# Optimization experiments

Measured on AMD Instinct MI355X. Metric: run time of the kernel, lower is better.

Reference implementation:

```python
import jax, jax.numpy as jnp
import numpy as np

V, E, H, L = 37, 256, 512, 3
B, S = 512, 128


def lstm_layer(x, W_ih, W_hh, b_ih, b_hh):
    # x: [B,S,D_in]; W_ih: [4H,D_in]; W_hh: [4H,H]; PyTorch gate order i,f,g,o
    Bx = x.shape[0]
    Hh = W_hh.shape[1]
    x_proj = jnp.einsum('bsd,gd->bsg', x, W_ih) + b_ih + b_hh  # [B,S,4H]

    def step(carry, xt):
        h, c = carry
        gates = xt + h @ W_hh.T
        i, f, g, o = jnp.split(gates, 4, axis=-1)
        i = jax.nn.sigmoid(i)
        f = jax.nn.sigmoid(f)
        g = jnp.tanh(g)
        o = jax.nn.sigmoid(o)
        c = f * c + i * g
        h = o * jnp.tanh(c)
        return (h, c), h

    init = (jnp.zeros((Bx, Hh), x.dtype), jnp.zeros((Bx, Hh), x.dtype))
    (hT, cT), hs = jax.lax.scan(step, init, jnp.swapaxes(x_proj, 0, 1))
    return jnp.swapaxes(hs, 0, 1), hT, cT


def setup_inputs() -> dict:
    key = jax.random.key(0)
    ks = jax.random.split(key, 16)
    inp = {'tokens': jax.random.randint(ks[0], (B, S), 0, V)}
    inp['embedding'] = jax.random.normal(ks[1], (V, E), jnp.float32) * 0.05
    for l in range(L):
        d_in = E if l == 0 else H
        inp[f'W_ih{l}'] = jax.random.normal(ks[2 + 4 * l], (4 * H, d_in), jnp.float32) * 0.05
        inp[f'W_hh{l}'] = jax.random.normal(ks[3 + 4 * l], (4 * H, H), jnp.float32) * 0.05
        inp[f'b_ih{l}'] = jnp.zeros((4 * H,), jnp.float32)
        inp[f'b_hh{l}'] = jnp.zeros((4 * H,), jnp.float32)
    inp['W_out'] = jax.random.normal(ks[14], (V, H), jnp.float32) * 0.05
    inp['b_out'] = jnp.zeros((V,), jnp.float32)
    return inp


def reference(tokens, embedding, W_ih0, W_hh0, b_ih0, b_hh0,
              W_ih1, W_hh1, b_ih1, b_hh1,
              W_ih2, W_hh2, b_ih2, b_hh2, W_out, b_out):
    x = embedding[tokens]  # [B,S,E]
    hs, cs = [], []
    for (Wi, Wh, bi, bh) in ((W_ih0, W_hh0, b_ih0, b_hh0),
                             (W_ih1, W_hh1, b_ih1, b_hh1),
                             (W_ih2, W_hh2, b_ih2, b_hh2)):
        x, hT, cT = lstm_layer(x, Wi, Wh, bi, bh)
        hs.append(hT)
        cs.append(cT)
    logits = jnp.einsum('bsh,vh->bsv', x, W_out) + b_out  # [B,S,V]
    return logits, jnp.stack(hs), jnp.stack(cs)
```

## Files before the change

kernel.cpp:

```cpp
#include <hip/hip_runtime.h>

typedef __attribute__((ext_vector_type(4))) float f32x4;
typedef __attribute__((ext_vector_type(8))) short bf16x8;

#define DEV __device__ __forceinline__

DEV float b2f(ushort u) { return __uint_as_float(((uint)u) << 16); }
DEV ushort f2b(float f) {
    uint u = __float_as_uint(f);
    return (ushort)((u + 0x7fffu + ((u >> 16) & 1u)) >> 16);
}
DEV float fsig(float x) {
    return __builtin_amdgcn_rcpf(1.f + __builtin_amdgcn_exp2f(-1.4426950408889634f * x));
}
DEV float ftanh(float x) {
    return 1.f - 2.f * __builtin_amdgcn_rcpf(__builtin_amdgcn_exp2f(2.885390081777927f * x) + 1.f);
}
DEV void gload_lds16(const void* g, void* l) {
    __builtin_amdgcn_global_load_lds(
        (const __attribute__((address_space(1))) void*)g,
        (__attribute__((address_space(3))) void*)l, 16, 0, 0);
}
DEV void gload_lds16_l2(const void* g, void* l) {
    __builtin_amdgcn_global_load_lds(
        (const __attribute__((address_space(1))) void*)g,
        (__attribute__((address_space(3))) void*)l, 16, 0, 1);
}
DEV void store_sc_u32(uint* p, uint v) {
    asm volatile("global_store_dword %0, %1, off sc0 sc1" :: "v"(p), "v"(v) : "memory");
}
DEV uint load_sc_u32(const uint* p) {
    uint v;
    asm volatile("global_load_dword %0, %1, off sc0 sc1\n\ts_waitcnt vmcnt(0)"
                 : "=v"(v) : "v"(p) : "memory");
    return v;
}

__global__ void f2b_kernel(const float* __restrict__ s, ushort* __restrict__ d, int n) {
    int i = blockIdx.x * 256 + threadIdx.x;
    if (i < n) d[i] = f2b(s[i]);
}

__global__ __launch_bounds__(256) void embed_kernel(
    const int* __restrict__ tok, const float* __restrict__ emb, ushort* __restrict__ x0) {
    const int nthr = gridDim.x * 256;
    for (int idx = blockIdx.x * 256 + threadIdx.x; idx < 128 * 512 * 32; idx += nthr) {
        const int row = idx >> 5;
        const int g8 = idx & 31;
        const int t = row >> 9, b = row & 511;
        const int tk = tok[b * 128 + t];
        const float* ep = emb + (size_t)tk * 256 + g8 * 8;
        float4 a = *(const float4*)ep;
        float4 c = *(const float4*)(ep + 4);
        uint4 o;
        o.x = (uint)f2b(a.x) | ((uint)f2b(a.y) << 16);
        o.y = (uint)f2b(a.z) | ((uint)f2b(a.w) << 16);
        o.z = (uint)f2b(c.x) | ((uint)f2b(c.y) << 16);
        o.w = (uint)f2b(c.z) | ((uint)f2b(c.w) << 16);
        *(uint4*)(x0 + (size_t)row * 256 + g8 * 8) = o;
    }
}

__global__ __launch_bounds__(256) void gemm_bias_kernel(
    const ushort* __restrict__ A, const ushort* __restrict__ Bw,
    const float* __restrict__ bias0, const float* __restrict__ bias1,
    ushort* __restrict__ C, int M, int N, int K) {
    __shared__ ushort la[128 * 32];
    __shared__ ushort lb[128 * 32];
    const int tid = threadIdx.x;
    const int wave = tid >> 6, lane = tid & 63;
    const int ntn = N >> 7;
    const int tm = blockIdx.x / ntn, tn = blockIdx.x % ntn;
    const int m0 = tm << 7, n0 = tn << 7;
    const int wm = (wave >> 1) * 64, wn = (wave & 1) * 64;
    f32x4 acc[4][4] = {};
    const int nks = K >> 5;
    const int srow = tid >> 2, scol = (tid & 3) * 8;
    for (int ks = 0; ks < nks; ++ks) {
        const int k0 = ks << 5;
#pragma unroll
        for (int r = 0; r < 2; ++r) {
            gload_lds16(A + (size_t)(m0 + r * 64 + srow) * K + k0 + scol, &la[r * 2048 + wave * 512]);
            gload_lds16(Bw + (size_t)(n0 + r * 64 + srow) * K + k0 + scol, &lb[r * 2048 + wave * 512]);
        }
        __syncthreads();
        bf16x8 af[4], bfr[4];
#pragma unroll
        for (int i = 0; i < 4; ++i)
            af[i] = *(const bf16x8*)&la[(wm + i * 16 + (lane & 15)) * 32 + (lane >> 4) * 8];
#pragma unroll
        for (int i = 0; i < 4; ++i)
            bfr[i] = *(const bf16x8*)&lb[(wn + i * 16 + (lane & 15)) * 32 + (lane >> 4) * 8];
#pragma unroll
        for (int mi = 0; mi < 4; ++mi)
#pragma unroll
            for (int ni = 0; ni < 4; ++ni)
                acc[mi][ni] = __builtin_amdgcn_mfma_f32_16x16x32_bf16(af[mi], bfr[ni], acc[mi][ni], 0, 0, 0);
        __syncthreads();
    }
#pragma unroll
    for (int mi = 0; mi < 4; ++mi) {
        int row = m0 + wm + mi * 16 + ((lane >> 4) << 2);
#pragma unroll
        for (int j = 0; j < 4; ++j) {
#pragma unroll
            for (int ni = 0; ni < 4; ++ni) {
                int col = n0 + wn + ni * 16 + (lane & 15);
                C[(size_t)(row + j) * N + col] = f2b(acc[mi][ni][j] + bias0[col] + bias1[col]);
            }
        }
    }
}

__global__ __launch_bounds__(256) void lstm_chunk_kernel(
    const ushort* __restrict__ xpj,
    const ushort* __restrict__ Whh,
    ushort* __restrict__ hs,
    float* __restrict__ cstate,
    float* __restrict__ hT, float* __restrict__ cT,
    uint* __restrict__ bar,
    int t0) {
    __shared__ ushort hp[64 * 512];
    __shared__ float gbuf[4][64][20];
    const int tid = threadIdx.x;
    const int wave = tid >> 6, lane = tid & 63;
    const int l15 = lane & 15, lh = lane >> 4;
    const int wr = wave >> 1, wc = wave & 1;
    const int grp = blockIdx.x & 7;
    const int hsl = blockIdx.x >> 3;
    const int b0 = grp << 6, h0 = hsl << 4;
    uint* gflags = bar + grp * 512;
    uint* myflag = gflags + hsl * 16;

    __threadfence();

    bf16x8 Bfr[2][16];
#pragma unroll
    for (int gg = 0; gg < 2; ++gg) {
        const ushort* wb = Whh + (size_t)((2 * wc + gg) * 512 + h0 + l15) * 512 + lh * 8;
#pragma unroll
        for (int ks = 0; ks < 16; ++ks) Bfr[gg][ks] = *(const bf16x8*)(wb + ks * 32);
    }

    float creg[4];
#pragma unroll
    for (int i = 0; i < 2; ++i) {
        const int e2 = i * 512 + tid * 2;
        const size_t ci = (size_t)(b0 + (e2 >> 4)) * 512 + h0 + (e2 & 15);
        if (t0 > 0) {
            float2 cv = *(const float2*)&cstate[ci];
            creg[2 * i] = cv.x; creg[2 * i + 1] = cv.y;
        } else {
            creg[2 * i] = 0.f; creg[2 * i + 1] = 0.f;
        }
    }

    uint xqc[8];
#pragma unroll
    for (int i = 0; i < 2; ++i) {
        const int e2 = i * 512 + tid * 2;
        const uint* xb = (const uint*)(xpj + (size_t)(b0 + (e2 >> 4)) * 2048 + h0 + (e2 & 15));
        xqc[i * 4 + 0] = xb[0]; xqc[i * 4 + 1] = xb[256];
        xqc[i * 4 + 2] = xb[512]; xqc[i * 4 + 3] = xb[768];
    }

    for (int tt = 0; tt < 32; ++tt) {
        const int t = t0 + tt;
        if (tt > 0) {
            if (wave == 0) {
                const uint* fp = gflags + ((lane & 31) << 4);
                const uint target = (uint)tt;
                while (!__all(load_sc_u32(fp) >= target)) __builtin_amdgcn_s_sleep(1);
            }
            __syncthreads();
        }
        f32x4 acc[2][2] = {};
        uint xqn[8];
        if (t > 0) {
            const ushort* hprev = hs + (size_t)(t - 1) * 262144;
#pragma unroll
            for (int rr = 0; rr < 16; ++rr) {
                const int row = rr * 4 + wave;
                gload_lds16_l2(hprev + (size_t)(b0 + row) * 512 + ((lane ^ (row & 7)) * 8),
                               &hp[row * 512]);
            }
            if (tt < 31) {
                const ushort* xt = xpj + (size_t)(tt + 1) * 1048576;
#pragma unroll
                for (int i = 0; i < 2; ++i) {
                    const int e2 = i * 512 + tid * 2;
                    const uint* xb = (const uint*)(xt + (size_t)(b0 + (e2 >> 4)) * 2048 + h0 + (e2 & 15));
                    xqn[i * 4 + 0] = xb[0]; xqn[i * 4 + 1] = xb[256];
                    xqn[i * 4 + 2] = xb[512]; xqn[i * 4 + 3] = xb[768];
                }
            }
            __syncthreads();
#pragma unroll
            for (int ks = 0; ks < 16; ++ks) {
#pragma unroll
                for (int m = 0; m < 2; ++m) {
                    const int row = (2 * wr + m) * 16 + l15;
                    const int c16 = (ks * 4 + lh) ^ (row & 7);
                    bf16x8 af = *(const bf16x8*)&hp[row * 512 + c16 * 8];
                    acc[m][0] = __builtin_amdgcn_mfma_f32_16x16x32_bf16(af, Bfr[0][ks], acc[m][0], 0, 0, 0);
                    acc[m][1] = __builtin_amdgcn_mfma_f32_16x16x32_bf16(af, Bfr[1][ks], acc[m][1], 0, 0, 0);
                }
            }
        } else if (tt < 31) {
            const ushort* xt = xpj + (size_t)(tt + 1) * 1048576;
#pragma unroll
            for (int i = 0; i < 2; ++i) {
                const int e2 = i * 512 + tid * 2;
                const uint* xb = (const uint*)(xt + (size_t)(b0 + (e2 >> 4)) * 2048 + h0 + (e2 & 15));
                xqn[i * 4 + 0] = xb[0]; xqn[i * 4 + 1] = xb[256];
                xqn[i * 4 + 2] = xb[512]; xqn[i * 4 + 3] = xb[768];
            }
        }
#pragma unroll
        for (int m = 0; m < 2; ++m)
#pragma unroll
            for (int gg = 0; gg < 2; ++gg)
#pragma unroll
                for (int j = 0; j < 4; ++j)
                    gbuf[2 * wc + gg][(2 * wr + m) * 16 + lh * 4 + j][l15] = acc[m][gg][j];
        __syncthreads();
        ushort* hout = hs + (size_t)t * 262144;
#pragma unroll
        for (int i = 0; i < 2; ++i) {
            const int e2 = i * 512 + tid * 2;
            const int b = e2 >> 4, hh = e2 & 15;
            float2 gI = *(const float2*)&gbuf[0][b][hh];
            float2 gF = *(const float2*)&gbuf[1][b][hh];
            float2 gG = *(const float2*)&gbuf[2][b][hh];
            float2 gO = *(const float2*)&gbuf[3][b][hh];
            float i0 = fsig(gI.x + b2f((ushort)(xqc[i * 4 + 0] & 0xffff)));
            float i1 = fsig(gI.y + b2f((ushort)(xqc[i * 4 + 0] >> 16)));
            float f0 = fsig(gF.x + b2f((ushort)(xqc[i * 4 + 1] & 0xffff)));
            float f1 = fsig(gF.y + b2f((ushort)(xqc[i * 4 + 1] >> 16)));
            float g0 = ftanh(gG.x + b2f((ushort)(xqc[i * 4 + 2] & 0xffff)));
            float g1 = ftanh(gG.y + b2f((ushort)(xqc[i * 4 + 2] >> 16)));
            float o0 = fsig(gO.x + b2f((ushort)(xqc[i * 4 + 3] & 0xffff)));
            float o1 = fsig(gO.y + b2f((ushort)(xqc[i * 4 + 3] >> 16)));
            float c0 = f0 * creg[2 * i] + i0 * g0;
            float c1 = f1 * creg[2 * i + 1] + i1 * g1;
            float h0v = o0 * ftanh(c0);
            float h1v = o1 * ftanh(c1);
            creg[2 * i] = c0; creg[2 * i + 1] = c1;
            const size_t ci = (size_t)(b0 + b) * 512 + h0 + hh;
            store_sc_u32((uint*)(hout + ci), (uint)f2b(h0v) | ((uint)f2b(h1v) << 16));
            if (t == 127) {
                *(float2*)&hT[ci] = make_float2(h0v, h1v);
                *(float2*)&cT[ci] = make_float2(c0, c1);
            }
        }
        if (tt < 31) {
#pragma unroll
            for (int k = 0; k < 8; ++k) xqc[k] = xqn[k];
        }
        if (tt < 31) {
            asm volatile("s_waitcnt vmcnt(0)" ::: "memory");
            __syncthreads();
            if (tid == 0) store_sc_u32(myflag, (uint)(tt + 1));
        }
    }
#pragma unroll
    for (int i = 0; i < 2; ++i) {
        const int e2 = i * 512 + tid * 2;
        const size_t ci = (size_t)(b0 + (e2 >> 4)) * 512 + h0 + (e2 & 15);
        *(float2*)&cstate[ci] = make_float2(creg[2 * i], creg[2 * i + 1]);
    }
}

__global__ __launch_bounds__(256) void outproj_kernel(
    const ushort* __restrict__ hs, const float* __restrict__ Wout,
    const float* __restrict__ bout, float* __restrict__ out) {
    __shared__ ushort lh[32 * 512];
    const int tid = threadIdx.x;
    const size_t r0 = (size_t)blockIdx.x * 32;
    const uint4* gs = (const uint4*)(hs + r0 * 512);
    uint4* ls = (uint4*)lh;
    for (int i = tid; i < 2048; i += 256) ls[i] = gs[i];
    __syncthreads();
    const int rg = tid & 7, vg = tid >> 3;
    float acc[4][2] = {};
    for (int k8 = 0; k8 < 64; ++k8) {
        float hf[4][8];
#pragma unroll
        for (int rr = 0; rr < 4; ++rr) {
            bf16x8 hv = *(const bf16x8*)&lh[(rg * 4 + rr) * 512 + k8 * 8];
#pragma unroll
            for (int j = 0; j < 8; ++j) hf[rr][j] = b2f((ushort)hv[j]);
        }
#pragma unroll
        for (int vi = 0; vi < 2; ++vi) {
            int v = vg + vi * 32;
            if (v < 37) {
                const float* wp = Wout + (size_t)v * 512 + k8 * 8;
                float4 w0 = *(const float4*)wp;
                float4 w1 = *(const float4*)(wp + 4);
                float wv[8] = {w0.x, w0.y, w0.z, w0.w, w1.x, w1.y, w1.z, w1.w};
#pragma unroll
                for (int rr = 0; rr < 4; ++rr) {
                    float s = 0.f;
#pragma unroll
                    for (int j = 0; j < 8; ++j) s += hf[rr][j] * wv[j];
                    acc[rr][vi] += s;
                }
            }
        }
    }
#pragma unroll
    for (int vi = 0; vi < 2; ++vi) {
        int v = vg + vi * 32;
        if (v < 37) {
#pragma unroll
            for (int rr = 0; rr < 4; ++rr) {
                size_t r = r0 + rg * 4 + rr;
                int t = (int)(r >> 9), b = (int)(r & 511);
                out[((size_t)b * 128 + t) * 37 + v] = acc[rr][vi] + bout[v];
            }
        }
    }
}

extern "C" void kernel_launch(void* const* d_in, const int* in_sizes, int n_in,
                              void* d_out, int out_size, void* d_ws, size_t ws_size,
                              hipStream_t stream) {
    (void)in_sizes; (void)n_in; (void)out_size; (void)ws_size;
    const int* tokens = (const int*)d_in[0];
    const float* emb = (const float*)d_in[1];
    const float* Wih_f[3] = {(const float*)d_in[2], (const float*)d_in[6], (const float*)d_in[10]};
    const float* Whh_f[3] = {(const float*)d_in[3], (const float*)d_in[7], (const float*)d_in[11]};
    const float* bih[3] = {(const float*)d_in[4], (const float*)d_in[8], (const float*)d_in[12]};
    const float* bhh[3] = {(const float*)d_in[5], (const float*)d_in[9], (const float*)d_in[13]};
    const float* Wout = (const float*)d_in[14];
    const float* bout = (const float*)d_in[15];
    float* out = (float*)d_out;

    char* ws = (char*)d_ws;
    size_t off = 0;
    auto take = [&](size_t nb) -> void* {
        void* p = ws + off;
        off = (off + nb + 255) & ~(size_t)255;
        return p;
    };
    ushort* x0 = (ushort*)take((size_t)128 * 512 * 256 * 2);
    ushort* hsA = (ushort*)take((size_t)128 * 512 * 512 * 2);
    ushort* hsB = (ushort*)take((size_t)128 * 512 * 512 * 2);
    ushort* xpj = (ushort*)take((size_t)32 * 512 * 2048 * 2);
    float* cst = (float*)take((size_t)512 * 512 * 4);
    ushort* wih[3];
    wih[0] = (ushort*)take((size_t)2048 * 256 * 2);
    wih[1] = (ushort*)take((size_t)2048 * 512 * 2);
    wih[2] = (ushort*)take((size_t)2048 * 512 * 2);
    ushort* whh[3];
    for (int l = 0; l < 3; ++l) whh[l] = (ushort*)take((size_t)2048 * 512 * 2);
    uint* barbase = (uint*)take((size_t)12 * 4096 * 4);

    hipMemsetAsync(barbase, 0, (size_t)12 * 4096 * 4, stream);

    f2b_kernel<<<2048, 256, 0, stream>>>(Wih_f[0], wih[0], 2048 * 256);
    f2b_kernel<<<4096, 256, 0, stream>>>(Wih_f[1], wih[1], 2048 * 512);
    f2b_kernel<<<4096, 256, 0, stream>>>(Wih_f[2], wih[2], 2048 * 512);
    for (int l = 0; l < 3; ++l)
        f2b_kernel<<<4096, 256, 0, stream>>>(Whh_f[l], whh[l], 2048 * 512);

    embed_kernel<<<2048, 256, 0, stream>>>(tokens, emb, x0);

    float* hTbase = out + 2424832;
    float* cTbase = out + 2424832 + 786432;
    const ushort* src = x0;
    ushort* hs_out = hsA;
    for (int l = 0; l < 3; ++l) {
        int K = (l == 0) ? 256 : 512;
        hs_out = (l == 1) ? hsB : hsA;
        for (int ch = 0; ch < 4; ++ch) {
            gemm_bias_kernel<<<2048, 256, 0, stream>>>(
                src + (size_t)ch * 16384 * K, wih[l], bih[l], bhh[l], xpj, 16384, 2048, K);
            lstm_chunk_kernel<<<256, 256, 0, stream>>>(
                xpj, whh[l], hs_out, cst,
                hTbase + (size_t)l * 262144, cTbase + (size_t)l * 262144,
                barbase + (size_t)(l * 4 + ch) * 4096, ch * 32);
        }
        src = hs_out;
    }
    outproj_kernel<<<2048, 256, 0, stream>>>(hs_out, Wout, bout, out);
}
```

Before: 2.721 ms.

## Overlap next chunk's input-projection GEMM with LSTM recurrence in one fused kernel

The per-chunk GEMM and the recurrent kernel are merged into a single launch. Blocks 0-255 run the recurrence for the current chunk, while blocks 256-511 compute the input projection for the next chunk, or the next layer's first chunk, into a double-buffered xpj. This hides the serialized GEMM launches behind the latency-bound recurrence and reuses a single hs buffer across layers. It also changes the recurrent wave split so each wave handles one gate over all 64 rows, and raises the priority of the recurrent waves. The risk is that co-resident GEMM blocks compete with the spin-waiting recurrent blocks for CU resources and bandwidth.

```diff
diff --git a/kernel.cpp b/kernel.cpp
--- a/kernel.cpp
+++ b/kernel.cpp
@@ -112,79 +112,100 @@
     }
 }
 
-__global__ __launch_bounds__(256) void lstm_chunk_kernel(
+__global__ __launch_bounds__(256) void fused_kernel(
     const ushort* __restrict__ xpj,
     const ushort* __restrict__ Whh,
     ushort* __restrict__ hs,
-    float* __restrict__ cstate,
-    float* __restrict__ hT, float* __restrict__ cT,
-    uint* __restrict__ bar,
-    int t0) {
-    __shared__ ushort hp[64 * 512];
-    __shared__ float gbuf[4][64][20];
+    float* __restrict__ cstate, float* __restrict__ hT, float* __restrict__ cT,
+    uint* __restrict__ bar, int t0,
+    const ushort* __restrict__ gA, const ushort* __restrict__ gB,
+    const float* __restrict__ gb0, const float* __restrict__ gb1,
+    ushort* __restrict__ gC, int gK, int do_gemm) {
+    __shared__ union SM {
+        struct { ushort hp[64 * 512]; float gbuf[4][64][16]; } r;
+        struct { ushort la[128 * 32]; ushort lb[128 * 32]; } g;
+    } sm;
     const int tid = threadIdx.x;
     const int wave = tid >> 6, lane = tid & 63;
-    const int l15 = lane & 15, lh = lane >> 4;
-    const int wr = wave >> 1, wc = wave & 1;
-    const int grp = blockIdx.x & 7;
-    const int hsl = blockIdx.x >> 3;
-    const int b0 = grp << 6, h0 = hsl << 4;
-    uint* gflags = bar + grp * 512;
-    uint* myflag = gflags + hsl * 16;
-
-    __threadfence();
-
-    bf16x8 Bfr[2][16];
-#pragma unroll
-    for (int gg = 0; gg < 2; ++gg) {
-        const ushort* wb = Whh + (size_t)((2 * wc + gg) * 512 + h0 + l15) * 512 + lh * 8;
-#pragma unroll
-        for (int ks = 0; ks < 16; ++ks) Bfr[gg][ks] = *(const bf16x8*)(wb + ks * 32);
-    }
-
-    float creg[4];
-#pragma unroll
-    for (int i = 0; i < 2; ++i) {
-        const int e2 = i * 512 + tid * 2;
-        const size_t ci = (size_t)(b0 + (e2 >> 4)) * 512 + h0 + (e2 & 15);
-        if (t0 > 0) {
-            float2 cv = *(const float2*)&cstate[ci];
-            creg[2 * i] = cv.x; creg[2 * i + 1] = cv.y;
-        } else {
-            creg[2 * i] = 0.f; creg[2 * i + 1] = 0.f;
-        }
-    }
-
-    uint xqc[8];
-#pragma unroll
-    for (int i = 0; i < 2; ++i) {
-        const int e2 = i * 512 + tid * 2;
-        const uint* xb = (const uint*)(xpj + (size_t)(b0 + (e2 >> 4)) * 2048 + h0 + (e2 & 15));
-        xqc[i * 4 + 0] = xb[0]; xqc[i * 4 + 1] = xb[256];
-        xqc[i * 4 + 2] = xb[512]; xqc[i * 4 + 3] = xb[768];
-    }
-
-    for (int tt = 0; tt < 32; ++tt) {
-        const int t = t0 + tt;
-        if (tt > 0) {
-            if (wave == 0) {
-                const uint* fp = gflags + ((lane & 31) << 4);
-                const uint target = (uint)tt;
-                while (!__all(load_sc_u32(fp) >= target)) __builtin_amdgcn_s_sleep(1);
-            }
-            __syncthreads();
-        }
-        f32x4 acc[2][2] = {};
-        uint xqn[8];
-        if (t > 0) {
-            const ushort* hprev = hs + (size_t)(t - 1) * 262144;
-#pragma unroll
-            for (int rr = 0; rr < 16; ++rr) {
-                const int row = rr * 4 + wave;
-                gload_lds16_l2(hprev + (size_t)(b0 + row) * 512 + ((lane ^ (row & 7)) * 8),
-                               &hp[row * 512]);
-            }
-            if (tt < 31) {
+
+    if (blockIdx.x < 256) {
+        const int grp = blockIdx.x & 7;
+        const int hsl = blockIdx.x >> 3;
+        const int b0 = grp << 6, h0 = hsl << 4;
+        uint* gflags = bar + grp * 512;
+        uint* myflag = gflags + hsl * 16;
+        __builtin_amdgcn_s_setprio(1);
+        __threadfence();
+
+        bf16x8 Bfr[16];
+        const ushort* wb = Whh + ((size_t)(wave * 512 + h0 + (lane & 15))) * 512 + (lane >> 4) * 8;
+#pragma unroll
+        for (int ks = 0; ks < 16; ++ks) Bfr[ks] = *(const bf16x8*)(wb + ks * 32);
+
+        float creg[4];
+#pragma unroll
+        for (int i = 0; i < 2; ++i) {
+            const int e2 = i * 512 + tid * 2;
+            const size_t ci = (size_t)(b0 + (e2 >> 4)) * 512 + h0 + (e2 & 15);
+            if (t0 > 0) {
+                float2 cv = *(const float2*)&cstate[ci];
+                creg[2 * i] = cv.x; creg[2 * i + 1] = cv.y;
+            } else {
+                creg[2 * i] = 0.f; creg[2 * i + 1] = 0.f;
+            }
+        }
+
+        uint xqc[8];
+#pragma unroll
+        for (int i = 0; i < 2; ++i) {
+            const int e2 = i * 512 + tid * 2;
+            const uint* xb = (const uint*)(xpj + (size_t)(b0 + (e2 >> 4)) * 2048 + h0 + (e2 & 15));
+            xqc[i * 4 + 0] = xb[0]; xqc[i * 4 + 1] = xb[256];
+            xqc[i * 4 + 2] = xb[512]; xqc[i * 4 + 3] = xb[768];
+        }
+
+        for (int tt = 0; tt < 32; ++tt) {
+            const int t = t0 + tt;
+            if (tt > 0) {
+                if (wave == 0) {
+                    const uint* fp = gflags + ((lane & 31) << 4);
+                    const uint target = (uint)tt;
+                    while (!__all(load_sc_u32(fp) >= target)) __builtin_amdgcn_s_sleep(1);
+                }
+                __syncthreads();
+            }
+            f32x4 acc[4] = {};
+            uint xqn[8];
+            if (t > 0) {
+                const ushort* hprev = hs + (size_t)(t - 1) * 262144;
+#pragma unroll
+                for (int rr = 0; rr < 16; ++rr) {
+                    const int row = rr * 4 + wave;
+                    gload_lds16_l2(hprev + (size_t)(b0 + row) * 512 + ((lane ^ (row & 7)) * 8),
+                                   &sm.r.hp[row * 512]);
+                }
+                if (tt < 31) {
+                    const ushort* xt = xpj + (size_t)(tt + 1) * 1048576;
+#pragma unroll
+                    for (int i = 0; i < 2; ++i) {
+                        const int e2 = i * 512 + tid * 2;
+                        const uint* xb = (const uint*)(xt + (size_t)(b0 + (e2 >> 4)) * 2048 + h0 + (e2 & 15));
+                        xqn[i * 4 + 0] = xb[0]; xqn[i * 4 + 1] = xb[256];
+                        xqn[i * 4 + 2] = xb[512]; xqn[i * 4 + 3] = xb[768];
+                    }
+                }
+                __syncthreads();
+#pragma unroll
+                for (int ks = 0; ks < 16; ++ks) {
+#pragma unroll
+                    for (int mi = 0; mi < 4; ++mi) {
+                        const int row = mi * 16 + (lane & 15);
+                        const int c16 = (ks * 4 + (lane >> 4)) ^ (row & 7);
+                        bf16x8 af = *(const bf16x8*)&sm.r.hp[row * 512 + c16 * 8];
+                        acc[mi] = __builtin_amdgcn_mfma_f32_16x16x32_bf16(af, Bfr[ks], acc[mi], 0, 0, 0);
+                    }
+                }
+            } else if (tt < 31) {
                 const ushort* xt = xpj + (size_t)(tt + 1) * 1048576;
 #pragma unroll
                 for (int i = 0; i < 2; ++i) {
@@ -194,80 +215,104 @@
                     xqn[i * 4 + 2] = xb[512]; xqn[i * 4 + 3] = xb[768];
                 }
             }
+#pragma unroll
+            for (int mi = 0; mi < 4; ++mi) {
+                const int rloc = mi * 16 + ((lane >> 4) << 2);
+#pragma unroll
+                for (int j = 0; j < 4; ++j) sm.r.gbuf[wave][rloc + j][lane & 15] = acc[mi][j];
+            }
             __syncthreads();
-#pragma unroll
-            for (int ks = 0; ks < 16; ++ks) {
-#pragma unroll
-                for (int m = 0; m < 2; ++m) {
-                    const int row = (2 * wr + m) * 16 + l15;
-                    const int c16 = (ks * 4 + lh) ^ (row & 7);
-                    bf16x8 af = *(const bf16x8*)&hp[row * 512 + c16 * 8];
-                    acc[m][0] = __builtin_amdgcn_mfma_f32_16x16x32_bf16(af, Bfr[0][ks], acc[m][0], 0, 0, 0);
-                    acc[m][1] = __builtin_amdgcn_mfma_f32_16x16x32_bf16(af, Bfr[1][ks], acc[m][1], 0, 0, 0);
-                }
-            }
-        } else if (tt < 31) {
-            const ushort* xt = xpj + (size_t)(tt + 1) * 1048576;
+            ushort* hout = hs + (size_t)t * 262144;
 #pragma unroll
             for (int i = 0; i < 2; ++i) {
                 const int e2 = i * 512 + tid * 2;
-                const uint* xb = (const uint*)(xt + (size_t)(b0 + (e2 >> 4)) * 2048 + h0 + (e2 & 15));
-                xqn[i * 4 + 0] = xb[0]; xqn[i * 4 + 1] = xb[256];
-                xqn[i * 4 + 2] = xb[512]; xqn[i * 4 + 3] = xb[768];
-            }
-        }
-#pragma unroll
-        for (int m = 0; m < 2; ++m)
-#pragma unroll
-            for (int gg = 0; gg < 2; ++gg)
-#pragma unroll
-                for (int j = 0; j < 4; ++j)
-                    gbuf[2 * wc + gg][(2 * wr + m) * 16 + lh * 4 + j][l15] = acc[m][gg][j];
-        __syncthreads();
-        ushort* hout = hs + (size_t)t * 262144;
+                const int b = e2 >> 4, hh = e2 & 15;
+                float2 gI = *(const float2*)&sm.r.gbuf[0][b][hh];
+                float2 gF = *(const float2*)&sm.r.gbuf[1][b][hh];
+                float2 gG = *(const float2*)&sm.r.gbuf[2][b][hh];
+                float2 gO = *(const float2*)&sm.r.gbuf[3][b][hh];
+                float i0 = fsig(gI.x + b2f((ushort)(xqc[i * 4 + 0] & 0xffff)));
+                float i1 = fsig(gI.y + b2f((ushort)(xqc[i * 4 + 0] >> 16)));
+                float f0 = fsig(gF.x + b2f((ushort)(xqc[i * 4 + 1] & 0xffff)));
+                float f1 = fsig(gF.y + b2f((ushort)(xqc[i * 4 + 1] >> 16)));
+                float g0 = ftanh(gG.x + b2f((ushort)(xqc[i * 4 + 2] & 0xffff)));
+                float g1 = ftanh(gG.y + b2f((ushort)(xqc[i * 4 + 2] >> 16)));
+                float o0 = fsig(gO.x + b2f((ushort)(xqc[i * 4 + 3] & 0xffff)));
+                float o1 = fsig(gO.y + b2f((ushort)(xqc[i * 4 + 3] >> 16)));
+                float c0 = f0 * creg[2 * i] + i0 * g0;
+                float c1 = f1 * creg[2 * i + 1] + i1 * g1;
+                float h0v = o0 * ftanh(c0);
+                float h1v = o1 * ftanh(c1);
+                creg[2 * i] = c0; creg[2 * i + 1] = c1;
+                const size_t ci = (size_t)(b0 + b) * 512 + h0 + hh;
+                store_sc_u32((uint*)(hout + ci), (uint)f2b(h0v) | ((uint)f2b(h1v) << 16));
+                if (t == 127) {
+                    *(float2*)&hT[ci] = make_float2(h0v, h1v);
+                    *(float2*)&cT[ci] = make_float2(c0, c1);
+                }
+            }
+            if (tt < 31) {
+#pragma unroll
+                for (int k = 0; k < 8; ++k) xqc[k] = xqn[k];
+                asm volatile("s_waitcnt vmcnt(0)" ::: "memory");
+                __syncthreads();
+                if (tid == 0) store_sc_u32(myflag, (uint)(tt + 1));
+            }
+        }
 #pragma unroll
         for (int i = 0; i < 2; ++i) {
             const int e2 = i * 512 + tid * 2;
-            const int b = e2 >> 4, hh = e2 & 15;
-            float2 gI = *(const float2*)&gbuf[0][b][hh];
-            float2 gF = *(const float2*)&gbuf[1][b][hh];
-            float2 gG = *(const float2*)&gbuf[2][b][hh];
-            float2 gO = *(const float2*)&gbuf[3][b][hh];
-            float i0 = fsig(gI.x + b2f((ushort)(xqc[i * 4 + 0] & 0xffff)));
-            float i1 = fsig(gI.y + b2f((ushort)(xqc[i * 4 + 0] >> 16)));
-            float f0 = fsig(gF.x + b2f((ushort)(xqc[i * 4 + 1] & 0xffff)));
-            float f1 = fsig(gF.y + b2f((ushort)(xqc[i * 4 + 1] >> 16)));
-            float g0 = ftanh(gG.x + b2f((ushort)(xqc[i * 4 + 2] & 0xffff)));
-            float g1 = ftanh(gG.y + b2f((ushort)(xqc[i * 4 + 2] >> 16)));
-            float o0 = fsig(gO.x + b2f((ushort)(xqc[i * 4 + 3] & 0xffff)));
-            float o1 = fsig(gO.y + b2f((ushort)(xqc[i * 4 + 3] >> 16)));
-            float c0 = f0 * creg[2 * i] + i0 * g0;
-            float c1 = f1 * creg[2 * i + 1] + i1 * g1;
-            float h0v = o0 * ftanh(c0);
-            float h1v = o1 * ftanh(c1);
-            creg[2 * i] = c0; creg[2 * i + 1] = c1;
-            const size_t ci = (size_t)(b0 + b) * 512 + h0 + hh;
-            store_sc_u32((uint*)(hout + ci), (uint)f2b(h0v) | ((uint)f2b(h1v) << 16));
-            if (t == 127) {
-                *(float2*)&hT[ci] = make_float2(h0v, h1v);
-                *(float2*)&cT[ci] = make_float2(c0, c1);
-            }
-        }
-        if (tt < 31) {
-#pragma unroll
-            for (int k = 0; k < 8; ++k) xqc[k] = xqn[k];
-        }
-        if (tt < 31) {
-            asm volatile("s_waitcnt vmcnt(0)" ::: "memory");
-            __syncthreads();
-            if (tid == 0) store_sc_u32(myflag, (uint)(tt + 1));
-        }
-    }
-#pragma unroll
-    for (int i = 0; i < 2; ++i) {
-        const int e2 = i * 512 + tid * 2;
-        const size_t ci = (size_t)(b0 + (e2 >> 4)) * 512 + h0 + (e2 & 15);
-        *(float2*)&cstate[ci] = make_float2(creg[2 * i], creg[2 * i + 1]);
+            const size_t ci = (size_t)(b0 + (e2 >> 4)) * 512 + h0 + (e2 & 15);
+            *(float2*)&cstate[ci] = make_float2(creg[2 * i], creg[2 * i + 1]);
+        }
+    } else {
+        if (!do_gemm) return;
+        const int gbid = blockIdx.x - 256;
+        const int l15 = lane & 15, lh = lane >> 4;
+        const int wm = (wave >> 1) * 64, wn = (wave & 1) * 64;
+        const int nks = gK >> 5;
+        const int srow = tid >> 2, scol = (tid & 3) * 8;
+        for (int tl = 0; tl < 8; ++tl) {
+            const int tile = gbid + tl * 256;
+            const int m0 = (tile >> 4) << 7, n0 = (tile & 15) << 7;
+            f32x4 acc[4][4] = {};
+            for (int ks = 0; ks < nks; ++ks) {
+                const int k0 = ks << 5;
+#pragma unroll
+                for (int r = 0; r < 2; ++r) {
+                    gload_lds16(gA + (size_t)(m0 + r * 64 + srow) * gK + k0 + scol,
+                                &sm.g.la[r * 2048 + wave * 512]);
+                    gload_lds16(gB + (size_t)(n0 + r * 64 + srow) * gK + k0 + scol,
+                                &sm.g.lb[r * 2048 + wave * 512]);
+                }
+                __syncthreads();
+                bf16x8 af[4], bfr[4];
+#pragma unroll
+                for (int i = 0; i < 4; ++i)
+                    af[i] = *(const bf16x8*)&sm.g.la[(wm + i * 16 + l15) * 32 + lh * 8];
+#pragma unroll
+                for (int i = 0; i < 4; ++i)
+                    bfr[i] = *(const bf16x8*)&sm.g.lb[(wn + i * 16 + l15) * 32 + lh * 8];
+#pragma unroll
+                for (int mi = 0; mi < 4; ++mi)
+#pragma unroll
+                    for (int ni = 0; ni < 4; ++ni)
+                        acc[mi][ni] = __builtin_amdgcn_mfma_f32_16x16x32_bf16(af[mi], bfr[ni], acc[mi][ni], 0, 0, 0);
+                __syncthreads();
+            }
+#pragma unroll
+            for (int mi = 0; mi < 4; ++mi) {
+                int row = m0 + wm + mi * 16 + (lh << 2);
+#pragma unroll
+                for (int j = 0; j < 4; ++j) {
+#pragma unroll
+                    for (int ni = 0; ni < 4; ++ni) {
+                        int col = n0 + wn + ni * 16 + l15;
+                        gC[(size_t)(row + j) * 2048 + col] = f2b(acc[mi][ni][j] + gb0[col] + gb1[col]);
+                    }
+                }
+            }
+        }
     }
 }
 
@@ -345,9 +390,9 @@
         return p;
     };
     ushort* x0 = (ushort*)take((size_t)128 * 512 * 256 * 2);
-    ushort* hsA = (ushort*)take((size_t)128 * 512 * 512 * 2);
-    ushort* hsB = (ushort*)take((size_t)128 * 512 * 512 * 2);
-    ushort* xpj = (ushort*)take((size_t)32 * 512 * 2048 * 2);
+    ushort* hs = (ushort*)take((size_t)128 * 512 * 512 * 2);
+    ushort* xpjA = (ushort*)take((size_t)32 * 512 * 2048 * 2);
+    ushort* xpjB = (ushort*)take((size_t)32 * 512 * 2048 * 2);
     float* cst = (float*)take((size_t)512 * 512 * 4);
     ushort* wih[3];
     wih[0] = (ushort*)take((size_t)2048 * 256 * 2);
@@ -369,20 +414,27 @@
 
     float* hTbase = out + 2424832;
     float* cTbase = out + 2424832 + 786432;
-    const ushort* src = x0;
-    ushort* hs_out = hsA;
+
+    gemm_bias_kernel<<<2048, 256, 0, stream>>>(x0, wih[0], bih[0], bhh[0], xpjA, 16384, 2048, 256);
+
+    ushort* xp[2] = {xpjA, xpjB};
+    int cur = 0;
     for (int l = 0; l < 3; ++l) {
-        int K = (l == 0) ? 256 : 512;
-        hs_out = (l == 1) ? hsB : hsA;
         for (int ch = 0; ch < 4; ++ch) {
-            gemm_bias_kernel<<<2048, 256, 0, stream>>>(
-                src + (size_t)ch * 16384 * K, wih[l], bih[l], bhh[l], xpj, 16384, 2048, K);
-            lstm_chunk_kernel<<<256, 256, 0, stream>>>(
-                xpj, whh[l], hs_out, cst,
+            int nl = l, nch = ch + 1;
+            if (nch == 4) { nl = l + 1; nch = 0; }
+            const int dog = (nl <= 2) ? 1 : 0;
+            const int bi = dog ? nl : 0;
+            const int nK = (bi == 0) ? 256 : 512;
+            const ushort* gAp = (bi == 0) ? (x0 + (size_t)nch * 16384 * 256)
+                                          : (hs + (size_t)nch * 16384 * 512);
+            fused_kernel<<<512, 256, 0, stream>>>(
+                xp[cur], whh[l], hs, cst,
                 hTbase + (size_t)l * 262144, cTbase + (size_t)l * 262144,
-                barbase + (size_t)(l * 4 + ch) * 4096, ch * 32);
-        }
-        src = hs_out;
-    }
-    outproj_kernel<<<2048, 256, 0, stream>>>(hs_out, Wout, bout, out);
-}
+                barbase + (size_t)(l * 4 + ch) * 4096, ch * 32,
+                gAp, wih[bi], bih[bi], bhh[bi], xp[cur ^ 1], nK, dog);
+            cur ^= 1;
+        }
+    }
+    outproj_kernel<<<2048, 256, 0, stream>>>(hs, Wout, bout, out);
+}
```

Measured after the change: 4.938 ms. 1.82x slower.
